# Optimization experiments

Measured on AMD Instinct MI355X. Metric: run time of the kernel, lower is better.

The kernel has to match this reference:

```python
import jax, jax.numpy as jnp
import numpy as np

N = 131072      # octree nodes at this depth
C_IN = 256      # in_channels == out_channels
C_B = 64        # bottleneck channels = out_channels // 4
K = 27          # 3x3x3 octree kernel neighborhood
EPS = 1e-5


def _bn(x, g, b, m, v):
    # inference-style BatchNorm with given running stats
    return (x - m) * (g * jax.lax.rsqrt(v + EPS)) + b


def setup_inputs() -> dict:
    key = jax.random.key(0)
    ks = jax.random.split(key, 20)
    inp = {
        "data": jax.random.normal(ks[0], (N, C_IN), dtype=jnp.float32),
        "neigh": jax.random.randint(ks[1], (N, K), 0, N, dtype=jnp.int32),
        "depth": 6,
        # conv1x1a (Linear, no bias) + BN
        "w1": jax.random.normal(ks[2], (C_IN, C_B), dtype=jnp.float32) * 0.05,
        "bn1_g": jax.random.uniform(ks[3], (C_B,), dtype=jnp.float32) + 0.5,
        "bn1_b": jax.random.normal(ks[4], (C_B,), dtype=jnp.float32) * 0.1,
        "bn1_m": jax.random.normal(ks[5], (C_B,), dtype=jnp.float32) * 0.1,
        "bn1_v": jax.random.uniform(ks[6], (C_B,), dtype=jnp.float32) + 0.5,
        # octree conv3x3 (27-neighbor gather + GEMM, no bias) + BN
        "w3": jax.random.normal(ks[7], (K, C_B, C_B), dtype=jnp.float32) * 0.02,
        "bn2_g": jax.random.uniform(ks[8], (C_B,), dtype=jnp.float32) + 0.5,
        "bn2_b": jax.random.normal(ks[9], (C_B,), dtype=jnp.float32) * 0.1,
        "bn2_m": jax.random.normal(ks[10], (C_B,), dtype=jnp.float32) * 0.1,
        "bn2_v": jax.random.uniform(ks[11], (C_B,), dtype=jnp.float32) + 0.5,
        # conv1x1b + BN (no ReLU)
        "w2": jax.random.normal(ks[12], (C_B, C_IN), dtype=jnp.float32) * 0.05,
        "bn3_g": jax.random.uniform(ks[13], (C_IN,), dtype=jnp.float32) + 0.5,
        "bn3_b": jax.random.normal(ks[14], (C_IN,), dtype=jnp.float32) * 0.1,
        "bn3_m": jax.random.normal(ks[15], (C_IN,), dtype=jnp.float32) * 0.1,
        "bn3_v": jax.random.uniform(ks[16], (C_IN,), dtype=jnp.float32) + 0.5,
    }
    return inp


def reference(data, neigh, depth, w1, bn1_g, bn1_b, bn1_m, bn1_v,
              w3, bn2_g, bn2_b, bn2_m, bn2_v,
              w2, bn3_g, bn3_b, bn3_m, bn3_v):
    # conv1x1a + BN + ReLU
    c1 = jax.nn.relu(_bn(data @ w1, bn1_g, bn1_b, bn1_m, bn1_v))  # [N, C_B]
    # octree conv3x3: gather 27 neighbors then contract with [K, C_B, C_B]
    gathered = c1[neigh]                                          # [N, K, C_B]
    c2 = jnp.einsum('nkc,kcd->nd', gathered, w3)                  # [N, C_B]
    c2 = jax.nn.relu(_bn(c2, bn2_g, bn2_b, bn2_m, bn2_v))
    # conv1x1b + BN (no relu)
    c3 = _bn(c2 @ w2, bn3_g, bn3_b, bn3_m, bn3_v)                 # [N, C_IN]
    # residual (in_channels == out_channels -> identity shortcut) + ReLU
    return jax.nn.relu(c3 + data)
```

## Files before the change

kernel.cpp:

```cpp
#include <hip/hip_runtime.h>

#define CIN 256
#define CB 64
#define KNB 27

typedef __attribute__((ext_vector_type(8))) short short8_t;
typedef __attribute__((ext_vector_type(4))) float f32x4;
typedef __attribute__((ext_vector_type(4))) int   i32x4;

__device__ inline unsigned short f2bf(float f) {
    union { float f; unsigned u; } x; x.f = f;
    unsigned r = x.u + 0x7fffu + ((x.u >> 16) & 1u);
    return (unsigned short)(r >> 16);
}
__device__ inline float bf2f(unsigned short h) {
    union { unsigned u; float f; } x; x.u = ((unsigned)h) << 16; return x.f;
}
__device__ inline f32x4 mfma16(short8_t a, short8_t b, f32x4 c) {
    return __builtin_amdgcn_mfma_f32_16x16x32_bf16(a, b, c, 0, 0, 0);
}
__device__ inline i32x4 mfma_i8(i32x4 a, i32x4 b, i32x4 c) {
    return __builtin_amdgcn_mfma_i32_16x16x64_i8(a, b, c, 0, 0, 0);
}

__global__ __launch_bounds__(256) void prep_a_kernel(
    const float* __restrict__ w1, const float* __restrict__ w2,
    const float* __restrict__ g1, const float* __restrict__ b1, const float* __restrict__ m1, const float* __restrict__ v1,
    const float* __restrict__ g2, const float* __restrict__ b2, const float* __restrict__ m2, const float* __restrict__ v2,
    const float* __restrict__ g3, const float* __restrict__ b3, const float* __restrict__ m3, const float* __restrict__ v3,
    unsigned short* __restrict__ w1p, unsigned short* __restrict__ w2p,
    float* __restrict__ bias1, float* __restrict__ bias2, float* __restrict__ bias3)
{
    int t = blockIdx.x * 256 + threadIdx.x;
    if (t < 16384) {
        int j = t & 7, lane = (t >> 3) & 63, tt = (t >> 9) & 3, s = t >> 11;
        int c = s * 32 + (lane >> 4) * 8 + j;
        int d = tt * 16 + (lane & 15);
        float sc = g1[d] * rsqrtf(v1[d] + 1e-5f);
        w1p[t] = f2bf(w1[c * CB + d] * sc);
    } else if (t < 32768) {
        int u = t - 16384;
        int j = u & 7, lane = (u >> 3) & 63, mt = (u >> 9) & 15, s = u >> 13;
        int c = s * 32 + (lane >> 4) * 8 + j;
        int d = mt * 16 + (lane & 15);
        float sc = g3[d] * rsqrtf(v3[d] + 1e-5f);
        w2p[u] = f2bf(w2[c * CIN + d] * sc);
    } else if (t < 33152) {
        int u = t - 32768;
        if (u < 64)       { float sc = g1[u] * rsqrtf(v1[u] + 1e-5f); bias1[u] = b1[u] - m1[u] * sc; }
        else if (u < 128) { int d = u - 64;  float sc = g2[d] * rsqrtf(v2[d] + 1e-5f); bias2[d] = b2[d] - m2[d] * sc; }
        else              { int d = u - 128; float sc = g3[d] * rsqrtf(v3[d] + 1e-5f); bias3[d] = b3[d] - m3[d] * sc; }
    }
}

__global__ __launch_bounds__(256) void prep_bq_kernel(
    const float* __restrict__ w3, const float* __restrict__ g2, const float* __restrict__ v2,
    signed char* __restrict__ w3q, unsigned* __restrict__ amax)
{
    __shared__ float sc2[64];
    __shared__ float sm[4];
    int tid = threadIdx.x;
    if (tid < 64) sc2[tid] = g2[tid] * rsqrtf(v2[tid] + 1e-5f);
    __syncthreads();

    const float4* w34 = (const float4*)w3;
    float m = 0.f;
    for (int e = tid; e < KNB * CB * CB / 4; e += 256) {
        float4 v = w34[e];
        int d0 = (e * 4) & 63;
        m = fmaxf(m, fabsf(v.x * sc2[d0]));
        m = fmaxf(m, fabsf(v.y * sc2[d0 + 1]));
        m = fmaxf(m, fabsf(v.z * sc2[d0 + 2]));
        m = fmaxf(m, fabsf(v.w * sc2[d0 + 3]));
    }
#pragma unroll
    for (int off = 32; off; off >>= 1) m = fmaxf(m, __shfl_xor(m, off));
    if ((tid & 63) == 0) sm[tid >> 6] = m;
    __syncthreads();
    float mm = fmaxf(fmaxf(sm[0], sm[1]), fmaxf(sm[2], sm[3]));
    float inv = mm > 0.f ? 127.f / mm : 0.f;

    int u = blockIdx.x * 256 + tid;
    int j = u & 15, lane = (u >> 4) & 63, tile = (u >> 10) & 3, k = u >> 12;
    int c = (lane >> 4) * 16 + j;
    int d = tile * 16 + (lane & 15);
    int q = __float2int_rn(w3[(k * CB + c) * CB + d] * sc2[d] * inv);
    q = q > 127 ? 127 : (q < -127 ? -127 : q);
    w3q[u] = (signed char)q;
    if (blockIdx.x == 0 && tid == 0) amax[1] = __float_as_uint(mm);
}

__global__ __launch_bounds__(256) void k1_conv1x1a(
    const float* __restrict__ data, const unsigned short* __restrict__ w1p,
    const float* __restrict__ bias1, unsigned short* __restrict__ c1b,
    float* __restrict__ blockmax)
{
    __shared__ short8_t w1s[2048];
    __shared__ float smax[4];
    int tid = threadIdx.x;
    const short8_t* wsrc = (const short8_t*)w1p;
#pragma unroll
    for (int i = 0; i < 8; i++) w1s[tid + i * 256] = wsrc[tid + i * 256];

    int lane = tid & 63, wave = tid >> 6;
    int g = lane >> 4, r = lane & 15;
    int rowbase = blockIdx.x * 128 + wave * 32;
    f32x4 acc[2][4] = {};
    __syncthreads();

#pragma unroll
    for (int s = 0; s < 8; s++) {
        short8_t a[2];
#pragma unroll
        for (int sub = 0; sub < 2; sub++) {
            const float* ap = data + (size_t)(rowbase + sub * 16 + r) * CIN + s * 32 + g * 8;
            float4 f0 = *(const float4*)ap;
            float4 f1 = *(const float4*)(ap + 4);
            short8_t av;
            av[0] = (short)f2bf(f0.x); av[1] = (short)f2bf(f0.y);
            av[2] = (short)f2bf(f0.z); av[3] = (short)f2bf(f0.w);
            av[4] = (short)f2bf(f1.x); av[5] = (short)f2bf(f1.y);
            av[6] = (short)f2bf(f1.z); av[7] = (short)f2bf(f1.w);
            a[sub] = av;
        }
#pragma unroll
        for (int t = 0; t < 4; t++) {
            short8_t b = w1s[(s * 4 + t) * 64 + lane];
            acc[0][t] = mfma16(a[0], b, acc[0][t]);
            acc[1][t] = mfma16(a[1], b, acc[1][t]);
        }
    }

    float mloc = 0.f;
#pragma unroll
    for (int sub = 0; sub < 2; sub++)
#pragma unroll
        for (int t = 0; t < 4; t++) {
            int col = t * 16 + r;
            float bs = bias1[col];
#pragma unroll
            for (int i = 0; i < 4; i++) {
                int row = rowbase + sub * 16 + g * 4 + i;
                float v = fmaxf(acc[sub][t][i] + bs, 0.f);
                mloc = fmaxf(mloc, v);
                c1b[row * CB + col] = f2bf(v);
            }
        }
#pragma unroll
    for (int off = 32; off; off >>= 1) mloc = fmaxf(mloc, __shfl_xor(mloc, off));
    if (lane == 0) smax[wave] = mloc;
    __syncthreads();
    if (tid == 0)
        blockmax[blockIdx.x] = fmaxf(fmaxf(smax[0], smax[1]), fmaxf(smax[2], smax[3]));
}

__global__ __launch_bounds__(256) void quant_c1_kernel(
    const unsigned short* __restrict__ c1b, const float* __restrict__ blockmax,
    signed char* __restrict__ c1q, unsigned* __restrict__ amax)
{
    __shared__ float sm[4];
    int tid = threadIdx.x;
    float4 bm = ((const float4*)blockmax)[tid];
    float m = fmaxf(fmaxf(bm.x, bm.y), fmaxf(bm.z, bm.w));
#pragma unroll
    for (int off = 32; off; off >>= 1) m = fmaxf(m, __shfl_xor(m, off));
    if ((tid & 63) == 0) sm[tid >> 6] = m;
    __syncthreads();
    float s1 = fmaxf(fmaxf(sm[0], sm[1]), fmaxf(sm[2], sm[3]));
    float inv = s1 > 0.f ? 127.f / s1 : 0.f;

    int t = blockIdx.x * 256 + tid;
    const short8_t* src = (const short8_t*)c1b;
    short8_t v0 = src[t * 2], v1 = src[t * 2 + 1];
    int ow[4];
#pragma unroll
    for (int h = 0; h < 4; h++) {
        int w = 0;
#pragma unroll
        for (int e = 0; e < 4; e++) {
            unsigned short hv = (unsigned short)((h < 2 ? v0 : v1)[(h & 1) * 4 + e]);
            int q = __float2int_rn(bf2f(hv) * inv);
            q = q > 127 ? 127 : q;
            w |= (q & 0xff) << (e * 8);
        }
        ow[h] = w;
    }
    ((int4*)c1q)[t] = make_int4(ow[0], ow[1], ow[2], ow[3]);
    if (blockIdx.x == 0 && tid == 0) amax[0] = __float_as_uint(s1);
}

__global__ __launch_bounds__(128, 6) void k2_conv3x3(
    const signed char* __restrict__ c1q, const int* __restrict__ neigh,
    const signed char* __restrict__ w3q, const float* __restrict__ bias2,
    const unsigned* __restrict__ amax, unsigned short* __restrict__ c2b)
{
    __shared__ int nidx[64 * KNB];
    int tid = threadIdx.x;
    int rowbase = blockIdx.x * 64;

    const int4* nsrc = (const int4*)(neigh + (size_t)rowbase * KNB);
#pragma unroll
    for (int i = 0; i < 4; i++) {
        int p = tid + i * 128;
        if (p < 432) ((int4*)nidx)[p] = nsrc[p];
    }

    int lane = tid & 63, wave = tid >> 6;
    int g = lane >> 4, r = lane & 15;
    int lr0 = wave * 32 + r, lr1 = wave * 32 + 16 + r;
    float sf = __uint_as_float(amax[0]) * __uint_as_float(amax[1]) * (1.f / (127.f * 127.f));
    __syncthreads();

    const i32x4* bq = (const i32x4*)w3q;
    i32x4 iacc[2][4] = {};

#pragma unroll
    for (int k = 0; k < KNB; k++) {
        i32x4 b0 = bq[k * 256 + lane];
        i32x4 b1 = bq[k * 256 + 64 + lane];
        i32x4 b2 = bq[k * 256 + 128 + lane];
        i32x4 b3 = bq[k * 256 + 192 + lane];
        int i0 = nidx[lr0 * KNB + k];
        int i1 = nidx[lr1 * KNB + k];
        i32x4 a0 = *(const i32x4*)(c1q + (size_t)i0 * CB + g * 16);
        i32x4 a1 = *(const i32x4*)(c1q + (size_t)i1 * CB + g * 16);
        iacc[0][0] = mfma_i8(a0, b0, iacc[0][0]);
        iacc[1][0] = mfma_i8(a1, b0, iacc[1][0]);
        iacc[0][1] = mfma_i8(a0, b1, iacc[0][1]);
        iacc[1][1] = mfma_i8(a1, b1, iacc[1][1]);
        iacc[0][2] = mfma_i8(a0, b2, iacc[0][2]);
        iacc[1][2] = mfma_i8(a1, b2, iacc[1][2]);
        iacc[0][3] = mfma_i8(a0, b3, iacc[0][3]);
        iacc[1][3] = mfma_i8(a1, b3, iacc[1][3]);
    }

#pragma unroll
    for (int sub = 0; sub < 2; sub++)
#pragma unroll
        for (int t = 0; t < 4; t++) {
            int col = t * 16 + r;
            float bs = bias2[col];
#pragma unroll
            for (int i = 0; i < 4; i++) {
                int row = rowbase + wave * 32 + sub * 16 + g * 4 + i;
                float v = fmaxf((float)iacc[sub][t][i] * sf + bs, 0.f);
                c2b[row * CB + col] = f2bf(v);
            }
        }
}

__global__ __launch_bounds__(256) void k3_conv1x1b(
    const unsigned short* __restrict__ c2b, const unsigned short* __restrict__ w2p,
    const float* __restrict__ bias3, const float* __restrict__ data,
    float* __restrict__ out)
{
    int tid = threadIdx.x;
    int lane = tid & 63, wave = tid >> 6;
    int g = lane >> 4, r = lane & 15;
    int rowbase = blockIdx.x * 64;

    const short8_t* abase = (const short8_t*)w2p;
    short8_t bfr[4][2];
#pragma unroll
    for (int sub = 0; sub < 4; sub++)
#pragma unroll
        for (int s = 0; s < 2; s++)
            bfr[sub][s] = *(const short8_t*)(c2b + (size_t)(rowbase + sub * 16 + r) * CB + s * 32 + g * 8);

    f32x4 acc2[4][4] = {};
#pragma unroll
    for (int s = 0; s < 2; s++)
#pragma unroll
        for (int mt = 0; mt < 4; mt++) {
            short8_t a = abase[(s * 16 + wave * 4 + mt) * 64 + lane];
#pragma unroll
            for (int sub = 0; sub < 4; sub++)
                acc2[sub][mt] = mfma16(a, bfr[sub][s], acc2[sub][mt]);
        }

#pragma unroll
    for (int sub = 0; sub < 4; sub++)
#pragma unroll
        for (int mt = 0; mt < 4; mt++) {
            int col0 = (wave * 4 + mt) * 16 + g * 4;
            int rowg = rowbase + sub * 16 + r;
            float4 bs = *(const float4*)(bias3 + col0);
            float4 dv = *(const float4*)(data + (size_t)rowg * CIN + col0);
            f32x4 v = acc2[sub][mt];
            float4 res;
            res.x = fmaxf(v[0] + bs.x + dv.x, 0.f);
            res.y = fmaxf(v[1] + bs.y + dv.y, 0.f);
            res.z = fmaxf(v[2] + bs.z + dv.z, 0.f);
            res.w = fmaxf(v[3] + bs.w + dv.w, 0.f);
            *(float4*)(out + (size_t)rowg * CIN + col0) = res;
        }
}

extern "C" void kernel_launch(void* const* d_in, const int* in_sizes, int n_in,
                              void* d_out, int out_size, void* d_ws, size_t ws_size,
                              hipStream_t stream)
{
    const float* data = (const float*)d_in[0];
    const int* neigh  = (const int*)d_in[1];
    const float* w1 = (const float*)d_in[3];
    const float* g1 = (const float*)d_in[4];
    const float* b1 = (const float*)d_in[5];
    const float* m1 = (const float*)d_in[6];
    const float* v1 = (const float*)d_in[7];
    const float* w3 = (const float*)d_in[8];
    const float* g2 = (const float*)d_in[9];
    const float* b2 = (const float*)d_in[10];
    const float* m2 = (const float*)d_in[11];
    const float* v2 = (const float*)d_in[12];
    const float* w2 = (const float*)d_in[13];
    const float* g3 = (const float*)d_in[14];
    const float* b3 = (const float*)d_in[15];
    const float* m3 = (const float*)d_in[16];
    const float* v3 = (const float*)d_in[17];
    float* out = (float*)d_out;

    char* ws = (char*)d_ws;
    unsigned short* c1b = (unsigned short*)ws;
    unsigned short* c2b = (unsigned short*)ws;
    signed char*    c1q = (signed char*)(ws + 16777216);
    unsigned short* w1p = (unsigned short*)(ws + 25165824);
    signed char*    w3q = (signed char*)(ws + 25198592);
    unsigned short* w2p = (unsigned short*)(ws + 25309184);
    float* bias1 = (float*)(ws + 25341952);
    float* bias2 = bias1 + 64;
    float* bias3 = bias1 + 128;
    unsigned* amax = (unsigned*)(ws + 25343488);
    float* blockmax = (float*)(ws + 25343552);

    int n = in_sizes[0] / CIN;

    hipLaunchKernelGGL(prep_a_kernel, dim3(130), dim3(256), 0, stream,
                       w1, w2, g1, b1, m1, v1, g2, b2, m2, v2, g3, b3, m3, v3,
                       w1p, w2p, bias1, bias2, bias3);
    hipLaunchKernelGGL(prep_bq_kernel, dim3(432), dim3(256), 0, stream,
                       w3, g2, v2, w3q, amax);
    hipLaunchKernelGGL(k1_conv1x1a, dim3(n / 128), dim3(256), 0, stream,
                       data, w1p, bias1, c1b, blockmax);
    hipLaunchKernelGGL(quant_c1_kernel, dim3(2048), dim3(256), 0, stream,
                       c1b, blockmax, c1q, amax);
    hipLaunchKernelGGL(k2_conv3x3, dim3(n / 64), dim3(128), 0, stream,
                       c1q, neigh, w3q, bias2, amax, c2b);
    hipLaunchKernelGGL(k3_conv1x1b, dim3(n / 64), dim3(256), 0, stream,
                       c2b, w2p, bias3, data, out);
}
```

Baseline: 207.7 us.

## Use single-wave conv3x3 blocks and stage conv1x1b epilogue through LDS for coalescing

The 3x3 octree conv kernel now launches one wave of 32 rows per block instead of two waves over 64 rows. This shrinks the shared neighbor-index tile and makes scheduling finer-grained. The final 1x1 conv epilogue first writes bias-added results into a padded LDS tile, then re-reads them row-contiguously. This allows fully coalesced float4 loads of the residual input and stores of the output. The cost is extra LDS traffic, a barrier and about 66KB of shared memory per block, which limits occupancy of that kernel.

```diff
diff --git a/kernel.cpp b/kernel.cpp
--- a/kernel.cpp
+++ b/kernel.cpp
@@ -189,25 +189,24 @@
     if (blockIdx.x == 0 && tid == 0) amax[0] = __float_as_uint(s1);
 }
 
-__global__ __launch_bounds__(128, 6) void k2_conv3x3(
+__global__ __launch_bounds__(64, 4) void k2_conv3x3(
     const signed char* __restrict__ c1q, const int* __restrict__ neigh,
     const signed char* __restrict__ w3q, const float* __restrict__ bias2,
     const unsigned* __restrict__ amax, unsigned short* __restrict__ c2b)
 {
-    __shared__ int nidx[64 * KNB];
-    int tid = threadIdx.x;
-    int rowbase = blockIdx.x * 64;
+    __shared__ int nidx[32 * KNB];
+    int tid = threadIdx.x;
+    int rowbase = blockIdx.x * 32;
 
     const int4* nsrc = (const int4*)(neigh + (size_t)rowbase * KNB);
 #pragma unroll
     for (int i = 0; i < 4; i++) {
-        int p = tid + i * 128;
-        if (p < 432) ((int4*)nidx)[p] = nsrc[p];
-    }
-
-    int lane = tid & 63, wave = tid >> 6;
+        int p = tid + i * 64;
+        if (p < 216) ((int4*)nidx)[p] = nsrc[p];
+    }
+
+    int lane = tid;
     int g = lane >> 4, r = lane & 15;
-    int lr0 = wave * 32 + r, lr1 = wave * 32 + 16 + r;
     float sf = __uint_as_float(amax[0]) * __uint_as_float(amax[1]) * (1.f / (127.f * 127.f));
     __syncthreads();
 
@@ -220,8 +219,8 @@
         i32x4 b1 = bq[k * 256 + 64 + lane];
         i32x4 b2 = bq[k * 256 + 128 + lane];
         i32x4 b3 = bq[k * 256 + 192 + lane];
-        int i0 = nidx[lr0 * KNB + k];
-        int i1 = nidx[lr1 * KNB + k];
+        int i0 = nidx[r * KNB + k];
+        int i1 = nidx[(16 + r) * KNB + k];
         i32x4 a0 = *(const i32x4*)(c1q + (size_t)i0 * CB + g * 16);
         i32x4 a1 = *(const i32x4*)(c1q + (size_t)i1 * CB + g * 16);
         iacc[0][0] = mfma_i8(a0, b0, iacc[0][0]);
@@ -242,7 +241,7 @@
             float bs = bias2[col];
 #pragma unroll
             for (int i = 0; i < 4; i++) {
-                int row = rowbase + wave * 32 + sub * 16 + g * 4 + i;
+                int row = rowbase + sub * 16 + g * 4 + i;
                 float v = fmaxf((float)iacc[sub][t][i] * sf + bs, 0.f);
                 c2b[row * CB + col] = f2bf(v);
             }
@@ -254,6 +253,7 @@
     const float* __restrict__ bias3, const float* __restrict__ data,
     float* __restrict__ out)
 {
+    __shared__ float otile[64 * 260];
     int tid = threadIdx.x;
     int lane = tid & 63, wave = tid >> 6;
     int g = lane >> 4, r = lane & 15;
@@ -283,17 +283,31 @@
 #pragma unroll
         for (int mt = 0; mt < 4; mt++) {
             int col0 = (wave * 4 + mt) * 16 + g * 4;
-            int rowg = rowbase + sub * 16 + r;
+            int lrow = sub * 16 + r;
             float4 bs = *(const float4*)(bias3 + col0);
-            float4 dv = *(const float4*)(data + (size_t)rowg * CIN + col0);
             f32x4 v = acc2[sub][mt];
-            float4 res;
-            res.x = fmaxf(v[0] + bs.x + dv.x, 0.f);
-            res.y = fmaxf(v[1] + bs.y + dv.y, 0.f);
-            res.z = fmaxf(v[2] + bs.z + dv.z, 0.f);
-            res.w = fmaxf(v[3] + bs.w + dv.w, 0.f);
-            *(float4*)(out + (size_t)rowg * CIN + col0) = res;
-        }
+            float4 sv;
+            sv.x = v[0] + bs.x; sv.y = v[1] + bs.y;
+            sv.z = v[2] + bs.z; sv.w = v[3] + bs.w;
+            *(float4*)&otile[lrow * 260 + col0] = sv;
+        }
+    __syncthreads();
+
+    const float4* dsrc = (const float4*)(data + (size_t)rowbase * CIN);
+    float4* dst = (float4*)(out + (size_t)rowbase * CIN);
+#pragma unroll
+    for (int p = 0; p < 16; p++) {
+        int idx = p * 256 + tid;
+        int row = idx >> 6, c4 = (idx & 63) << 2;
+        float4 ov = *(const float4*)&otile[row * 260 + c4];
+        float4 dv = dsrc[idx];
+        float4 res;
+        res.x = fmaxf(ov.x + dv.x, 0.f);
+        res.y = fmaxf(ov.y + dv.y, 0.f);
+        res.z = fmaxf(ov.z + dv.z, 0.f);
+        res.w = fmaxf(ov.w + dv.w, 0.f);
+        dst[idx] = res;
+    }
 }
 
 extern "C" void kernel_launch(void* const* d_in, const int* in_sizes, int n_in,
@@ -343,7 +357,7 @@
                        data, w1p, bias1, c1b, blockmax);
     hipLaunchKernelGGL(quant_c1_kernel, dim3(2048), dim3(256), 0, stream,
                        c1b, blockmax, c1q, amax);
-    hipLaunchKernelGGL(k2_conv3x3, dim3(n / 64), dim3(128), 0, stream,
+    hipLaunchKernelGGL(k2_conv3x3, dim3(n / 32), dim3(64), 0, stream,
                        c1q, neigh, w3q, bias2, amax, c2b);
     hipLaunchKernelGGL(k3_conv1x1b, dim3(n / 64), dim3(256), 0, stream,
                        c2b, w2p, bias3, data, out);
```

Result: faster. 175.6 us, median of 2 (-15.4%).
